# Optimization experiments

Hardware: AMD Instinct MI355X
Metric: run time of the kernel (lower is better)

Reference implementation:

```python
import jax, jax.numpy as jnp
import numpy as np
from jax import lax

EPS_BN = 1e-5
EPS_LN = 1e-5
PATCH = 16

def _gelu(x):
    return jax.nn.gelu(x, approximate=False)

def _patch(x, cw, cb, pw, pb):
    # x: [B, C, H, W]; conv stride=kernel=PATCH -> [B, C, 14, 14]
    y = lax.conv_general_dilated(x, cw, (PATCH, PATCH), 'VALID',
                                 dimension_numbers=('NCHW', 'OIHW', 'NCHW'))
    y = y + cb[None, :, None, None]
    y = y.reshape(y.shape[0], y.shape[1], -1)          # b c (h w) = [B, C, 196]
    return jnp.einsum('bcn,ln->bcl', y, pw) + pb        # Linear(196 -> 256)

def _bn_c(y, g, b, rm, rv):
    # eval-mode BatchNorm over channel axis=1 of [B, C, L]
    inv = g / jnp.sqrt(rv + EPS_BN)
    return y * inv[None, :, None] + (b - rm * inv)[None, :, None]

def _cross(x1, x2, w, b, g, beta, rm, rv):
    c = jnp.concatenate([x1, x2], axis=1)               # [B, 2P, L]
    y = lax.conv_general_dilated(c, w, (1,), ((1, 1),),
                                 dimension_numbers=('NCH', 'OIH', 'NCH'))
    y = y + b[None, :, None]
    return _gelu(_bn_c(y, g, beta, rm, rv))

def _mamba(x, Win, cw, cb, Wx, Wdt, bdt, Alog, Dp, Wout):
    # Standard mamba_ssm Mamba block, eval mode. x: [B, L, D]
    Di = Win.shape[0] // 2
    N = Alog.shape[1]
    R = Wdt.shape[1]
    Bsz, L, _ = x.shape
    xz = jnp.einsum('bld,ed->ble', x, Win)              # in_proj (no bias)
    xc, z = xz[..., :Di], xz[..., Di:]
    K = cw.shape[1]
    xp = jnp.pad(xc, ((0, 0), (K - 1, 0), (0, 0)))      # causal depthwise conv
    xconv = cb + sum(xp[:, k:k + L, :] * cw[:, k] for k in range(K))
    xc = jax.nn.silu(xconv)
    dbc = jnp.einsum('bld,ed->ble', xc, Wx)             # x_proj
    dt = jax.nn.softplus(jnp.einsum('blr,dr->bld', dbc[..., :R], Wdt) + bdt)
    Bm = dbc[..., R:R + N]
    Cm = dbc[..., R + N:]
    A = -jnp.exp(Alog)                                  # [Di, N]
    def step(h, inp):
        dt_t, b_t, c_t, x_t = inp                       # [B,Di],[B,N],[B,N],[B,Di]
        h = jnp.exp(dt_t[:, :, None] * A) * h + dt_t[:, :, None] * b_t[:, None, :] * x_t[:, :, None]
        return h, jnp.einsum('bdn,bn->bd', h, c_t)
    h0 = jnp.zeros((Bsz, Di, N), x.dtype)
    _, ys = lax.scan(step, h0, (dt.swapaxes(0, 1), Bm.swapaxes(0, 1), Cm.swapaxes(0, 1), xc.swapaxes(0, 1)))
    y = ys.swapaxes(0, 1) + Dp * xc
    y = y * jax.nn.silu(z)
    return jnp.einsum('bld,od->blo', y, Wout)           # out_proj (no bias)

def _mamba_stack(x, p):
    # residual stack: x = mamba_i(x) + x
    for i in range(p[0].shape[0]):
        x = _mamba(x, *(q[i] for q in p)) + x
    return x

def _forward(x_cwt, y_cwt, z_cwt,
             x_conv_w, x_conv_b, x_proj_w, x_proj_b,
             y_conv_w, y_conv_b, y_proj_w, y_proj_b,
             z_conv_w, z_conv_b, z_proj_w, z_proj_b,
             cc_w, cc_b, cc_g, cc_beta, cc_rm, cc_rv,
             fu_w, fu_b, fu_g, fu_beta, fu_rm, fu_rv,
             ln_g, ln_b,
             m1_in_w, m1_conv_w, m1_conv_b, m1_x_w, m1_dt_w, m1_dt_b, m1_Alog, m1_D, m1_out_w,
             m2_in_w, m2_conv_w, m2_conv_b, m2_x_w, m2_dt_w, m2_dt_b, m2_Alog, m2_D, m2_out_w,
             cl1_w, cl1_b, cl2_w, cl2_b):
    xr = _gelu(_patch(x_cwt, x_conv_w, x_conv_b, x_proj_w, x_proj_b)).swapaxes(1, 2)  # [B,256,32]
    yr = _gelu(_patch(y_cwt, y_conv_w, y_conv_b, y_proj_w, y_proj_b)).swapaxes(1, 2)
    zr = _gelu(_patch(z_cwt, z_conv_w, z_conv_b, z_proj_w, z_proj_b)).swapaxes(1, 2)
    cxy = _cross(xr, yr, cc_w, cc_b, cc_g, cc_beta, cc_rm, cc_rv)
    cxz = _cross(xr, zr, cc_w, cc_b, cc_g, cc_beta, cc_rm, cc_rv)
    cyz = _cross(yr, zr, cc_w, cc_b, cc_g, cc_beta, cc_rm, cc_rv)
    # max_pooling == 0 -> mean pooling over last dim
    feats = jnp.concatenate([xr.mean(2), yr.mean(2), zr.mean(2),
                             cxy.mean(2), cxz.mean(2), cyz.mean(2)], axis=1)  # [B,1536]
    f = feats @ fu_w.T + fu_b
    inv = fu_g / jnp.sqrt(fu_rv + EPS_BN)
    f = _gelu(f * inv + (fu_beta - fu_rm * inv))        # BN1d eval + GELU (dropout=eval identity)
    xf = f[:, None, :]                                  # [B, 1, 256]
    mu = xf.mean(-1, keepdims=True)
    var = ((xf - mu) ** 2).mean(-1, keepdims=True)
    xf = (xf - mu) / jnp.sqrt(var + EPS_LN) * ln_g + ln_b
    m1 = (m1_in_w, m1_conv_w, m1_conv_b, m1_x_w, m1_dt_w, m1_dt_b, m1_Alog, m1_D, m1_out_w)
    m2 = (m2_in_w, m2_conv_w, m2_conv_b, m2_x_w, m2_dt_w, m2_dt_b, m2_Alog, m2_D, m2_out_w)
    # branch 1: scan over (trivial) time axis, bidirectional, reverse_flip == 1
    x1 = _mamba_stack(xf, m1)
    x1f = _mamba_stack(jnp.flip(xf, axis=1), m1)
    x1 = x1 + jnp.flip(x1f, axis=1)
    # branch 2: scan over feature axis (permuted), bidirectional
    xperm = x1.swapaxes(1, 2)                           # [B, 256, 1]
    x2 = _mamba_stack(xperm, m2)
    x2f = _mamba_stack(jnp.flip(xperm, axis=1), m2)
    x2f = x2f.swapaxes(1, 2)                            # [B, 1, 256]
    x2 = x2.swapaxes(1, 2) + jnp.flip(x2f, axis=1)
    x3 = (x2 + x1)[:, 0, :]                             # squeeze(1)
    h = x3 @ cl1_w.T + cl1_b
    return h @ cl2_w.T + cl2_b

def setup_inputs():
    key = jax.random.key(0)
    ks = iter(jax.random.split(key, 80))
    rn = lambda *s: jax.random.normal(next(ks), s, jnp.float32) * 0.05
    d = {}
    d['x_cwt'] = jax.random.normal(next(ks), (32, 32, 224, 224), jnp.float32)
    d['y_cwt'] = jax.random.normal(next(ks), (32, 32, 224, 224), jnp.float32)
    d['z_cwt'] = jax.random.normal(next(ks), (32, 32, 224, 224), jnp.float32)
    for s in ('x', 'y', 'z'):
        d[s + '_conv_w'] = rn(32, 32, 16, 16)
        d[s + '_conv_b'] = jnp.zeros((32,), jnp.float32)
        d[s + '_proj_w'] = rn(256, 196)
        d[s + '_proj_b'] = jnp.zeros((256,), jnp.float32)
    d['cc_w'] = rn(256, 512, 3); d['cc_b'] = jnp.zeros((256,)); d['cc_g'] = jnp.ones((256,))
    d['cc_beta'] = jnp.zeros((256,)); d['cc_rm'] = jnp.zeros((256,)); d['cc_rv'] = jnp.ones((256,))
    d['fu_w'] = rn(256, 1536); d['fu_b'] = jnp.zeros((256,)); d['fu_g'] = jnp.ones((256,))
    d['fu_beta'] = jnp.zeros((256,)); d['fu_rm'] = jnp.zeros((256,)); d['fu_rv'] = jnp.ones((256,))
    d['ln_g'] = jnp.ones((256,)); d['ln_b'] = jnp.zeros((256,))
    alog = jnp.log(jnp.arange(1, 17, dtype=jnp.float32))
    d['m1_in_w'] = rn(2, 1024, 256); d['m1_conv_w'] = rn(2, 512, 4); d['m1_conv_b'] = jnp.zeros((2, 512))
    d['m1_x_w'] = rn(2, 48, 512); d['m1_dt_w'] = rn(2, 512, 16); d['m1_dt_b'] = jnp.zeros((2, 512))
    d['m1_Alog'] = jnp.broadcast_to(alog, (2, 512, 16)) + 0.0; d['m1_D'] = jnp.ones((2, 512)); d['m1_out_w'] = rn(2, 256, 512)
    d['m2_in_w'] = rn(2, 4, 1); d['m2_conv_w'] = rn(2, 2, 4); d['m2_conv_b'] = jnp.zeros((2, 2))
    d['m2_x_w'] = rn(2, 33, 2); d['m2_dt_w'] = rn(2, 2, 1); d['m2_dt_b'] = jnp.zeros((2, 2))
    d['m2_Alog'] = jnp.broadcast_to(alog, (2, 2, 16)) + 0.0; d['m2_D'] = jnp.ones((2, 2)); d['m2_out_w'] = rn(2, 1, 2)
    d['cl1_w'] = rn(128, 256); d['cl1_b'] = jnp.zeros((128,))
    d['cl2_w'] = rn(18, 128); d['cl2_b'] = jnp.zeros((18,))
    return d

def reference(x_cwt, y_cwt, z_cwt,
              x_conv_w, x_conv_b, x_proj_w, x_proj_b,
              y_conv_w, y_conv_b, y_proj_w, y_proj_b,
              z_conv_w, z_conv_b, z_proj_w, z_proj_b,
              cc_w, cc_b, cc_g, cc_beta, cc_rm, cc_rv,
              fu_w, fu_b, fu_g, fu_beta, fu_rm, fu_rv,
              ln_g, ln_b,
              m1_in_w, m1_conv_w, m1_conv_b, m1_x_w, m1_dt_w, m1_dt_b, m1_Alog, m1_D, m1_out_w,
              m2_in_w, m2_conv_w, m2_conv_b, m2_x_w, m2_dt_w, m2_dt_b, m2_Alog, m2_D, m2_out_w,
              cl1_w, cl1_b, cl2_w, cl2_b):
    return _forward(x_cwt, y_cwt, z_cwt,
                    x_conv_w, x_conv_b, x_proj_w, x_proj_b,
                    y_conv_w, y_conv_b, y_proj_w, y_proj_b,
                    z_conv_w, z_conv_b, z_proj_w, z_proj_b,
                    cc_w, cc_b, cc_g, cc_beta, cc_rm, cc_rv,
                    fu_w, fu_b, fu_g, fu_beta, fu_rm, fu_rv,
                    ln_g, ln_b,
                    m1_in_w, m1_conv_w, m1_conv_b, m1_x_w, m1_dt_w, m1_dt_b, m1_Alog, m1_D, m1_out_w,
                    m2_in_w, m2_conv_w, m2_conv_b, m2_x_w, m2_dt_w, m2_dt_b, m2_Alog, m2_D, m2_out_w,
                    cl1_w, cl1_b, cl2_w, cl2_b)
```

## Files before the change

kernel.cpp:

```cpp
#include <hip/hip_runtime.h>
#include <math.h>


__device__ __forceinline__ float gelu_f(float x) {
    return 0.5f * x * (1.0f + erff(x * 0.70710678118654752f));
}
__device__ __forceinline__ float silu_f(float x) {
    return x / (1.0f + expf(-x));
}
__device__ __forceinline__ float softplus_f(float x) {
    return (x > 20.0f) ? x : log1pf(expf(x));
}

__global__ __launch_bounds__(256, 2)
void k_patch_conv(const float* __restrict__ X0, const float* __restrict__ X1, const float* __restrict__ X2,
                  const float* __restrict__ W0, const float* __restrict__ W1, const float* __restrict__ W2,
                  const float* __restrict__ B0, const float* __restrict__ B1, const float* __restrict__ B2,
                  float* __restrict__ P) {
    int bid = blockIdx.x;
    int s = bid / 448; int rem = bid % 448; int b = rem / 14; int ph = rem % 14;
    const float* X  = (s == 0) ? X0 : ((s == 1) ? X1 : X2);
    const float* W  = (s == 0) ? W0 : ((s == 1) ? W1 : W2);
    const float* Bb = (s == 0) ? B0 : ((s == 1) ? B1 : B2);

    __shared__ float4 xs4[16 * 57];
    __shared__ float4 ws4[32 * 64];
    __shared__ float  red[16 * 112];

    int tid = threadIdx.x;
    int ij = tid & 3;
    int i  = ij & 1;
    int j  = ij >> 1;
    int k  = tid >> 2;
    int kh = k >> 2;
    int kwq = k & 3;

    float acc[7][16];
#pragma unroll
    for (int p = 0; p < 7; ++p) {
#pragma unroll
        for (int c = 0; c < 16; ++c) acc[p][c] = 0.f;
    }

    for (int ci = 0; ci < 32; ++ci) {
        __syncthreads();
        const float4* xg = (const float4*)(X + ((size_t)(b * 32 + ci)) * 50176 + (size_t)ph * 3584);
        for (int t = tid; t < 896; t += 256) {
            int r = t / 56, c4 = t % 56;
            xs4[r * 57 + c4] = xg[t];
        }
        const float4* wg = (const float4*)W;
        for (int t = tid; t < 2048; t += 256) {
            int co = t >> 6, q = t & 63;
            ws4[t] = wg[(size_t)(co * 32 + ci) * 64 + q];
        }
        __syncthreads();

        float4 xv[7];
        const float4* xr_ = &xs4[kh * 57 + i * 28 + kwq];
#pragma unroll
        for (int p = 0; p < 7; ++p) xv[p] = xr_[p * 4];
#pragma unroll
        for (int c = 0; c < 16; ++c) {
            float4 wv = ws4[(j * 16 + c) * 64 + k];
#pragma unroll
            for (int p = 0; p < 7; ++p) {
                acc[p][c] += xv[p].x * wv.x + xv[p].y * wv.y + xv[p].z * wv.z + xv[p].w * wv.w;
            }
        }
    }

#pragma unroll
    for (int p = 0; p < 7; ++p) {
#pragma unroll
        for (int c = 0; c < 16; ++c) {
            float v = acc[p][c];
            v += __shfl_xor(v, 4);
            v += __shfl_xor(v, 8);
            v += __shfl_xor(v, 16);
            v += __shfl_xor(v, 32);
            acc[p][c] = v;
        }
    }
    int wave = tid >> 6, lane = tid & 63;
    if (lane < 4) {
#pragma unroll
        for (int p = 0; p < 7; ++p) {
#pragma unroll
            for (int c = 0; c < 16; ++c) {
                red[(wave * 4 + lane) * 112 + p * 16 + c] = acc[p][c];
            }
        }
    }
    __syncthreads();
    for (int t = tid; t < 448; t += 256) {
        int ij2 = t / 112, v = t % 112;
        int p = v / 16, c = v % 16;
        float sum = red[(0 * 4 + ij2) * 112 + v] + red[(1 * 4 + ij2) * 112 + v] +
                    red[(2 * 4 + ij2) * 112 + v] + red[(3 * 4 + ij2) * 112 + v];
        int pw = (ij2 & 1) * 7 + p;
        int co = (ij2 >> 1) * 16 + c;
        P[(((size_t)s * 32 + b) * 32 + co) * 196 + ph * 14 + pw] = sum + Bb[co];
    }
}

__global__ __launch_bounds__(128)
void k_proj(const float* __restrict__ P,
            const float* __restrict__ PW0, const float* __restrict__ PW1, const float* __restrict__ PW2,
            const float* __restrict__ PB0, const float* __restrict__ PB1, const float* __restrict__ PB2,
            float* __restrict__ R, float* __restrict__ feats) {
    int bid = blockIdx.x;
    int s = bid / 64; int r2 = bid % 64; int b = r2 >> 1; int half = r2 & 1;
    const float* PW = (s == 0) ? PW0 : ((s == 1) ? PW1 : PW2);
    const float* PB = (s == 0) ? PB0 : ((s == 1) ? PB1 : PB2);

    __shared__ float4 ps4[32 * 49];
    const float4* src = (const float4*)(P + ((size_t)s * 32 + b) * 6272);
    for (int t = threadIdx.x; t < 1568; t += 128) ps4[t] = src[t];
    __syncthreads();

    int l = half * 128 + threadIdx.x;
    float acc[32];
#pragma unroll
    for (int c = 0; c < 32; ++c) acc[c] = 0.f;

    const float4* pwl = (const float4*)(PW + (size_t)l * 196);
    for (int n4 = 0; n4 < 49; ++n4) {
        float4 pv = pwl[n4];
#pragma unroll
        for (int c = 0; c < 32; ++c) {
            float4 xv = ps4[c * 49 + n4];
            acc[c] += pv.x * xv.x + pv.y * xv.y + pv.z * xv.z + pv.w * xv.w;
        }
    }
    float pbl = PB[l];
    float m = 0.f;
    float* Rrow = R + (((size_t)s * 32 + b) * 256 + l) * 32;
#pragma unroll
    for (int c = 0; c < 32; ++c) {
        float v = gelu_f(acc[c] + pbl);
        Rrow[c] = v;
        m += v;
    }
    feats[b * 1536 + s * 256 + l] = m * 0.03125f;
}

__global__ __launch_bounds__(256)
void k_cross(const float* __restrict__ R, const float* __restrict__ CCW,
             const float* __restrict__ CCB, const float* __restrict__ CCG,
             const float* __restrict__ CCBETA, const float* __restrict__ CCRM,
             const float* __restrict__ CCRV, float* __restrict__ feats) {
    int b = blockIdx.x >> 3, cs = blockIdx.x & 7;
    int c0 = cs * 4;
    __shared__ float ls[3 * 256 * 8];
    for (int t = threadIdx.x; t < 4608; t += 256) {
        int ten = t / 1536; int r2 = t % 1536; int r = r2 / 6; int cc = r2 % 6;
        int cg = c0 - 1 + cc;
        float v = 0.f;
        if (cg >= 0 && cg < 32) v = R[(((size_t)ten * 32 + b) * 256 + r) * 32 + cg];
        ls[(ten * 256 + r) * 8 + cc] = v;
    }
    __syncthreads();

    int o = threadIdx.x;
    float a1[4] = {0, 0, 0, 0}, a2[4] = {0, 0, 0, 0}, a3[4] = {0, 0, 0, 0};
    const float* wrow = CCW + (size_t)o * 1536;

    for (int ii = 0; ii < 256; ++ii) {
        float w0 = wrow[ii * 3], w1 = wrow[ii * 3 + 1], w2 = wrow[ii * 3 + 2];
        const float* U = &ls[(0 * 256 + ii) * 8];
        const float* V = &ls[(1 * 256 + ii) * 8];
#pragma unroll
        for (int c = 0; c < 4; ++c) {
            float su_ = w0 * U[c] + w1 * U[c + 1] + w2 * U[c + 2];
            float sv_ = w0 * V[c] + w1 * V[c + 1] + w2 * V[c + 2];
            a1[c] += su_; a2[c] += su_; a3[c] += sv_;
        }
    }
    for (int ii = 0; ii < 256; ++ii) {
        float w0 = wrow[768 + ii * 3], w1 = wrow[768 + ii * 3 + 1], w2 = wrow[768 + ii * 3 + 2];
        const float* U = &ls[(1 * 256 + ii) * 8];
        const float* V = &ls[(2 * 256 + ii) * 8];
#pragma unroll
        for (int c = 0; c < 4; ++c) {
            float su_ = w0 * U[c] + w1 * U[c + 1] + w2 * U[c + 2];
            float sv_ = w0 * V[c] + w1 * V[c + 1] + w2 * V[c + 2];
            a1[c] += su_; a2[c] += sv_; a3[c] += sv_;
        }
    }

    float inv = CCG[o] / sqrtf(CCRV[o] + 1e-5f);
    float sh = CCBETA[o] - CCRM[o] * inv;
    float bias = CCB[o];
    float s1 = 0.f, s2 = 0.f, s3 = 0.f;
#pragma unroll
    for (int c = 0; c < 4; ++c) {
        s1 += gelu_f((a1[c] + bias) * inv + sh);
        s2 += gelu_f((a2[c] + bias) * inv + sh);
        s3 += gelu_f((a3[c] + bias) * inv + sh);
    }
    float* fb = feats + b * 1536 + 768;
    atomicAdd(&fb[o],       s1 * 0.03125f);
    atomicAdd(&fb[256 + o], s2 * 0.03125f);
    atomicAdd(&fb[512 + o], s3 * 0.03125f);
}

__global__ __launch_bounds__(256)
void k_fuse(const float* __restrict__ feats, const float* __restrict__ FUW, const float* __restrict__ FUB,
            const float* __restrict__ FUG, const float* __restrict__ FUBETA, const float* __restrict__ FURM,
            const float* __restrict__ FURV, const float* __restrict__ LNG, const float* __restrict__ LNB,
            float* __restrict__ xf) {
    int b = blockIdx.x;
    __shared__ float4 sf4[384];
    const float4* src = (const float4*)(feats + (size_t)b * 1536);
    for (int t = threadIdx.x; t < 384; t += 256) sf4[t] = src[t];
    __syncthreads();

    int o = threadIdx.x;
    const float4* wr = (const float4*)(FUW + (size_t)o * 1536);
    float acc = 0.f;
    for (int q = 0; q < 384; ++q) {
        float4 wv = wr[q], xv = sf4[q];
        acc += wv.x * xv.x + wv.y * xv.y + wv.z * xv.z + wv.w * xv.w;
    }
    float inv = FUG[o] / sqrtf(FURV[o] + 1e-5f);
    float f = (acc + FUB[o]) * inv + (FUBETA[o] - FURM[o] * inv);
    f = gelu_f(f);

    float s1 = f, s2 = f * f;
#pragma unroll
    for (int off = 32; off >= 1; off >>= 1) {
        s1 += __shfl_xor(s1, off);
        s2 += __shfl_xor(s2, off);
    }
    __shared__ float wred[8];
    int wave = threadIdx.x >> 6, lane = threadIdx.x & 63;
    if (lane == 0) { wred[wave * 2] = s1; wred[wave * 2 + 1] = s2; }
    __syncthreads();
    float mu  = (wred[0] + wred[2] + wred[4] + wred[6]) * (1.f / 256.f);
    float ex2 = (wred[1] + wred[3] + wred[5] + wred[7]) * (1.f / 256.f);
    float var = ex2 - mu * mu;
    xf[b * 256 + o] = (f - mu) / sqrtf(var + 1e-5f) * LNG[o] + LNB[o];
}

__global__ __launch_bounds__(256)
void k_m1(const float* __restrict__ Uin, float* __restrict__ Uout,
          const float* __restrict__ WIN, const float* __restrict__ CW, const float* __restrict__ CB,
          const float* __restrict__ WX, const float* __restrict__ WDT, const float* __restrict__ BDT,
          const float* __restrict__ DP, const float* __restrict__ WOUT, int layer) {
    const float* Win  = WIN  + (size_t)layer * 1024 * 256;
    const float* cw   = CW   + layer * 2048;
    const float* cb   = CB   + layer * 512;
    const float* Wx   = WX   + layer * 48 * 512;
    const float* Wdt  = WDT  + layer * 512 * 16;
    const float* bdt  = BDT  + layer * 512;
    const float* Dp   = DP   + layer * 512;
    const float* Wout = WOUT + layer * 256 * 512;

    int b = blockIdx.x, tid = threadIdx.x;
    __shared__ float su[256];
    __shared__ float sz[1024];
    __shared__ float sx[512];
    __shared__ float sdbc[48];
    __shared__ float sy[512];

    su[tid] = Uin[b * 256 + tid];
    __syncthreads();

    const float4* su4 = (const float4*)su;
#pragma unroll
    for (int q = 0; q < 4; ++q) {
        int e = tid + q * 256;
        const float4* wr = (const float4*)(Win + (size_t)e * 256);
        float acc = 0.f;
        for (int t = 0; t < 64; ++t) {
            float4 wv = wr[t], xv = su4[t];
            acc += wv.x * xv.x + wv.y * xv.y + wv.z * xv.z + wv.w * xv.w;
        }
        sz[e] = acc;
    }
    __syncthreads();
#pragma unroll
    for (int q = 0; q < 2; ++q) {
        int d = tid + q * 256;
        sx[d] = silu_f(cb[d] + sz[d] * cw[d * 4 + 3]);
    }
    __syncthreads();
    if (tid < 48) {
        const float4* wr = (const float4*)(Wx + (size_t)tid * 512);
        const float4* sx4 = (const float4*)sx;
        float acc = 0.f;
        for (int t = 0; t < 128; ++t) {
            float4 wv = wr[t], xv = sx4[t];
            acc += wv.x * xv.x + wv.y * xv.y + wv.z * xv.z + wv.w * xv.w;
        }
        sdbc[tid] = acc;
    }
    __syncthreads();
    float bc = 0.f;
#pragma unroll
    for (int n = 0; n < 16; ++n) bc += sdbc[16 + n] * sdbc[32 + n];
#pragma unroll
    for (int q = 0; q < 2; ++q) {
        int d = tid + q * 256;
        float dtin = 0.f;
#pragma unroll
        for (int r = 0; r < 16; ++r) dtin += sdbc[r] * Wdt[d * 16 + r];
        float dtv = softplus_f(dtin + bdt[d]);
        float xcv = sx[d];
        float y = dtv * xcv * bc + Dp[d] * xcv;
        y *= silu_f(sz[512 + d]);
        sy[d] = y;
    }
    __syncthreads();
    {
        const float4* wr = (const float4*)(Wout + (size_t)tid * 512);
        const float4* sy4 = (const float4*)sy;
        float acc = 0.f;
        for (int t = 0; t < 128; ++t) {
            float4 wv = wr[t], xv = sy4[t];
            acc += wv.x * xv.x + wv.y * xv.y + wv.z * xv.z + wv.w * xv.w;
        }
        Uout[b * 256 + tid] = acc + su[tid];
    }
}

__global__ __launch_bounds__(256)
void k_m2(const float* __restrict__ SRC, float* __restrict__ DST, int first,
          const float* __restrict__ WIN, const float* __restrict__ CW, const float* __restrict__ CB,
          const float* __restrict__ WX, const float* __restrict__ WDT, const float* __restrict__ BDT,
          const float* __restrict__ ALOG, const float* __restrict__ DP, const float* __restrict__ WOUT,
          int layer) {
    const float* Win  = WIN  + layer * 4;
    const float* cw   = CW   + layer * 8;
    const float* cb   = CB   + layer * 2;
    const float* Wx   = WX   + layer * 66;
    const float* Wdt  = WDT  + layer * 2;
    const float* bdt  = BDT  + layer * 2;
    const float* Alog = ALOG + layer * 32;
    const float* Dp   = DP   + layer * 2;
    const float* Wout = WOUT + layer * 2;

    int v = blockIdx.x, b = v >> 1, dir = v & 1, l = threadIdx.x;
    __shared__ float sxc[256 * 2];
    __shared__ float sC[256 * 16];
    __shared__ float suu[256 * 32];
    __shared__ float sdt[256 * 2];
    __shared__ float sy[256 * 2];

    float u;
    if (first) u = 2.f * SRC[b * 256 + (dir ? (255 - l) : l)];
    else       u = SRC[v * 256 + l];

    float xc0 = u * Win[0], xc1 = u * Win[1];
    float z0  = u * Win[2], z1  = u * Win[3];
    sxc[l * 2 + 0] = xc0; sxc[l * 2 + 1] = xc1;
    __syncthreads();

    float xs0, xs1;
    {
        float a0 = cb[0], a1 = cb[1];
#pragma unroll
        for (int kk = 0; kk < 4; ++kk) {
            int lk = l - 3 + kk;
            if (lk >= 0) {
                a0 += sxc[lk * 2 + 0] * cw[kk];
                a1 += sxc[lk * 2 + 1] * cw[4 + kk];
            }
        }
        xs0 = silu_f(a0); xs1 = silu_f(a1);
    }
    float dbc0 = xs0 * Wx[0] + xs1 * Wx[1];
    float dt0 = softplus_f(dbc0 * Wdt[0] + bdt[0]);
    float dt1 = softplus_f(dbc0 * Wdt[1] + bdt[1]);
    sdt[l * 2 + 0] = dt0; sdt[l * 2 + 1] = dt1;
#pragma unroll
    for (int n = 0; n < 16; ++n) {
        float Bn = xs0 * Wx[(1 + n) * 2] + xs1 * Wx[(1 + n) * 2 + 1];
        float Cn = xs0 * Wx[(17 + n) * 2] + xs1 * Wx[(17 + n) * 2 + 1];
        sC[l * 16 + n] = Cn;
        suu[l * 32 + n]      = dt0 * Bn * xs0;
        suu[l * 32 + 16 + n] = dt1 * Bn * xs1;
    }
    __syncthreads();

    if (l < 32) {
        int d = l >> 4, n = l & 15;
        float A = -expf(Alog[d * 16 + n]);
        float h = 0.f;
#pragma unroll 4
        for (int t = 0; t < 256; ++t) {
            float a = expf(sdt[t * 2 + d] * A);
            h = a * h + suu[t * 32 + l];
            float part = h * sC[t * 16 + n];
            part += __shfl_xor(part, 1);
            part += __shfl_xor(part, 2);
            part += __shfl_xor(part, 4);
            part += __shfl_xor(part, 8);
            if (n == 0) sy[t * 2 + d] = part;
        }
    }
    __syncthreads();
    {
        float y0 = sy[l * 2 + 0] + Dp[0] * xs0;
        float y1 = sy[l * 2 + 1] + Dp[1] * xs1;
        y0 *= silu_f(z0); y1 *= silu_f(z1);
        DST[v * 256 + l] = y0 * Wout[0] + y1 * Wout[1] + u;
    }
}

__global__ __launch_bounds__(256)
void k_final(const float* __restrict__ M2b, const float* __restrict__ XF1,
             const float* __restrict__ CL1W, const float* __restrict__ CL1B,
             const float* __restrict__ CL2W, const float* __restrict__ CL2B,
             float* __restrict__ out) {
    int b = blockIdx.x, tid = threadIdx.x;
    __shared__ float sx3[256];
    __shared__ float shh[128];
    sx3[tid] = M2b[(2 * b) * 256 + tid] + M2b[(2 * b + 1) * 256 + tid] + 2.f * XF1[b * 256 + tid];
    __syncthreads();
    if (tid < 128) {
        const float4* wr = (const float4*)(CL1W + (size_t)tid * 256);
        const float4* x4 = (const float4*)sx3;
        float acc = 0.f;
        for (int t = 0; t < 64; ++t) {
            float4 wv = wr[t], xv = x4[t];
            acc += wv.x * xv.x + wv.y * xv.y + wv.z * xv.z + wv.w * xv.w;
        }
        shh[tid] = acc + CL1B[tid];
    }
    __syncthreads();
    if (tid < 18) {
        const float4* wr = (const float4*)(CL2W + (size_t)tid * 128);
        const float4* h4 = (const float4*)shh;
        float acc = 0.f;
        for (int t = 0; t < 32; ++t) {
            float4 wv = wr[t], xv = h4[t];
            acc += wv.x * xv.x + wv.y * xv.y + wv.z * xv.z + wv.w * xv.w;
        }
        out[b * 18 + tid] = acc + CL2B[tid];
    }
}


#define DI(i) ((const float*)d_in[i])

extern "C" void kernel_launch(void* const* d_in, const int* in_sizes, int n_in,
                              void* d_out, int out_size, void* d_ws, size_t ws_size,
                              hipStream_t stream) {
    float* ws    = (float*)d_ws;
    float* P     = ws;
    float* R     = P + 602112;
    float* feats = R + 786432;
    float* xf    = feats + 49152;
    float* U1    = xf + 8192;
    float* XF1   = U1 + 8192;
    float* M2a   = XF1 + 8192;
    float* M2b   = M2a + 16384;

    hipMemsetAsync(feats, 0, 49152 * sizeof(float), stream);

    k_patch_conv<<<1344, 256, 0, stream>>>(DI(0), DI(1), DI(2),
                                           DI(3), DI(7), DI(11),
                                           DI(4), DI(8), DI(12), P);
    k_proj<<<192, 128, 0, stream>>>(P, DI(5), DI(9), DI(13), DI(6), DI(10), DI(14), R, feats);
    k_cross<<<256, 256, 0, stream>>>(R, DI(15), DI(16), DI(17), DI(18), DI(19), DI(20), feats);
    k_fuse<<<32, 256, 0, stream>>>(feats, DI(21), DI(22), DI(23), DI(24), DI(25), DI(26),
                                   DI(27), DI(28), xf);
    k_m1<<<32, 256, 0, stream>>>(xf, U1, DI(29), DI(30), DI(31), DI(32), DI(33), DI(34),
                                 DI(36), DI(37), 0);
    k_m1<<<32, 256, 0, stream>>>(U1, XF1, DI(29), DI(30), DI(31), DI(32), DI(33), DI(34),
                                 DI(36), DI(37), 1);
    k_m2<<<64, 256, 0, stream>>>(XF1, M2a, 1, DI(38), DI(39), DI(40), DI(41), DI(42), DI(43),
                                 DI(44), DI(45), DI(46), 0);
    k_m2<<<64, 256, 0, stream>>>(M2a, M2b, 0, DI(38), DI(39), DI(40), DI(41), DI(42), DI(43),
                                 DI(44), DI(45), DI(46), 1);
    k_final<<<32, 256, 0, stream>>>(M2b, XF1, DI(47), DI(48), DI(49), DI(50), (float*)d_out);
}
```

Before: 1.439 ms.

## Double-buffer patch conv via direct global-to-LDS loads and pretranspose weights for coalescing

```diff
diff --git a/kernel.cpp b/kernel.cpp
--- a/kernel.cpp
+++ b/kernel.cpp
@@ -10,6 +10,40 @@
 }
 __device__ __forceinline__ float softplus_f(float x) {
     return (x > 20.0f) ? x : log1pf(expf(x));
+}
+
+__device__ __forceinline__ void gl2lds(const float4* g, float4* l) {
+    __builtin_amdgcn_global_load_lds((const __attribute__((address_space(1))) void*)g,
+                                     (__attribute__((address_space(3))) void*)l,
+                                     16, 0, 0);
+}
+
+__global__ __launch_bounds__(256)
+void k_tr(const float* __restrict__ src, float* __restrict__ dst, int R, int C) {
+    __shared__ float t[32][33];
+    int ctiles = C >> 5;
+    int bx = blockIdx.x % ctiles, by = blockIdx.x / ctiles;
+    int c0 = bx * 32, r0 = by * 32;
+    int tx = threadIdx.x & 31, ty = threadIdx.x >> 5;
+#pragma unroll
+    for (int k = 0; k < 4; ++k) {
+        int r = ty + k * 8;
+        t[r][tx] = src[(size_t)(r0 + r) * C + c0 + tx];
+    }
+    __syncthreads();
+#pragma unroll
+    for (int k = 0; k < 4; ++k) {
+        int r = ty + k * 8;
+        dst[(size_t)(c0 + r) * R + r0 + tx] = t[tx][r];
+    }
+}
+
+__global__ __launch_bounds__(256)
+void k_p4(const float* __restrict__ src, float4* __restrict__ dst, int E, int Dq) {
+    int idx = blockIdx.x * 256 + threadIdx.x;
+    if (idx >= E * Dq) return;
+    int e = idx / Dq, dq = idx % Dq;
+    dst[(size_t)dq * E + e] = *(const float4*)(src + (size_t)e * 4 * Dq + 4 * dq);
 }
 
 __global__ __launch_bounds__(256, 2)
@@ -23,11 +57,12 @@
     const float* W  = (s == 0) ? W0 : ((s == 1) ? W1 : W2);
     const float* Bb = (s == 0) ? B0 : ((s == 1) ? B1 : B2);
 
-    __shared__ float4 xs4[16 * 57];
-    __shared__ float4 ws4[32 * 64];
+    __shared__ float4 xs4[2][1024];
+    __shared__ float4 ws4[2048];
     __shared__ float  red[16 * 112];
 
     int tid = threadIdx.x;
+    int wave = tid >> 6, lane = tid & 63;
     int ij = tid & 3;
     int i  = ij & 1;
     int j  = ij >> 1;
@@ -35,29 +70,45 @@
     int kh = k >> 2;
     int kwq = k & 3;
 
+    const float4* xg = (const float4*)X + (size_t)(b * 32) * 12544 + ph * 896;
+    const float4* wg = (const float4*)W;
+
+#pragma unroll
+    for (int q = 0; q < 4; ++q) {
+        int chunk = wave * 4 + q;
+        int idx = chunk * 64 + lane; if (idx > 895) idx = 895;
+        gl2lds(xg + idx, &xs4[0][chunk * 64]);
+    }
+
     float acc[7][16];
 #pragma unroll
-    for (int p = 0; p < 7; ++p) {
+    for (int p = 0; p < 7; ++p)
 #pragma unroll
         for (int c = 0; c < 16; ++c) acc[p][c] = 0.f;
-    }
 
     for (int ci = 0; ci < 32; ++ci) {
-        __syncthreads();
-        const float4* xg = (const float4*)(X + ((size_t)(b * 32 + ci)) * 50176 + (size_t)ph * 3584);
-        for (int t = tid; t < 896; t += 256) {
-            int r = t / 56, c4 = t % 56;
-            xs4[r * 57 + c4] = xg[t];
-        }
-        const float4* wg = (const float4*)W;
-        for (int t = tid; t < 2048; t += 256) {
-            int co = t >> 6, q = t & 63;
-            ws4[t] = wg[(size_t)(co * 32 + ci) * 64 + q];
-        }
-        __syncthreads();
-
+        asm volatile("s_barrier" ::: "memory");
+#pragma unroll
+        for (int q = 0; q < 8; ++q) {
+            int c = wave * 8 + q;
+            gl2lds(wg + (size_t)c * 2048 + ci * 64 + lane, &ws4[c * 64]);
+        }
+        if (ci < 31) {
+            const float4* xgn = xg + (size_t)(ci + 1) * 12544;
+#pragma unroll
+            for (int q = 0; q < 4; ++q) {
+                int chunk = wave * 4 + q;
+                int idx = chunk * 64 + lane; if (idx > 895) idx = 895;
+                gl2lds(xgn + idx, &xs4[(ci + 1) & 1][chunk * 64]);
+            }
+            asm volatile("s_waitcnt vmcnt(4)" ::: "memory");
+        } else {
+            asm volatile("s_waitcnt vmcnt(0)" ::: "memory");
+        }
+        asm volatile("s_barrier" ::: "memory");
+
+        const float4* xr_ = &xs4[ci & 1][kh * 56 + i * 28 + kwq];
         float4 xv[7];
-        const float4* xr_ = &xs4[kh * 57 + i * 28 + kwq];
 #pragma unroll
         for (int p = 0; p < 7; ++p) xv[p] = xr_[p * 4];
 #pragma unroll
@@ -82,15 +133,12 @@
             acc[p][c] = v;
         }
     }
-    int wave = tid >> 6, lane = tid & 63;
     if (lane < 4) {
 #pragma unroll
-        for (int p = 0; p < 7; ++p) {
-#pragma unroll
-            for (int c = 0; c < 16; ++c) {
+        for (int p = 0; p < 7; ++p)
+#pragma unroll
+            for (int c = 0; c < 16; ++c)
                 red[(wave * 4 + lane) * 112 + p * 16 + c] = acc[p][c];
-            }
-        }
     }
     __syncthreads();
     for (int t = tid; t < 448; t += 256) {
@@ -105,16 +153,15 @@
 }
 
 __global__ __launch_bounds__(128)
-void k_proj(const float* __restrict__ P,
-            const float* __restrict__ PW0, const float* __restrict__ PW1, const float* __restrict__ PW2,
+void k_proj(const float* __restrict__ P, const float4* __restrict__ PWP,
             const float* __restrict__ PB0, const float* __restrict__ PB1, const float* __restrict__ PB2,
             float* __restrict__ R, float* __restrict__ feats) {
     int bid = blockIdx.x;
     int s = bid / 64; int r2 = bid % 64; int b = r2 >> 1; int half = r2 & 1;
-    const float* PW = (s == 0) ? PW0 : ((s == 1) ? PW1 : PW2);
     const float* PB = (s == 0) ? PB0 : ((s == 1) ? PB1 : PB2);
-
-    __shared__ float4 ps4[32 * 49];
+    const float4* pwp = PWP + (size_t)s * 12544;
+
+    __shared__ __align__(16) float4 ps4[32 * 49];
     const float4* src = (const float4*)(P + ((size_t)s * 32 + b) * 6272);
     for (int t = threadIdx.x; t < 1568; t += 128) ps4[t] = src[t];
     __syncthreads();
@@ -124,9 +171,8 @@
 #pragma unroll
     for (int c = 0; c < 32; ++c) acc[c] = 0.f;
 
-    const float4* pwl = (const float4*)(PW + (size_t)l * 196);
     for (int n4 = 0; n4 < 49; ++n4) {
-        float4 pv = pwl[n4];
+        float4 pv = pwp[n4 * 256 + l];
 #pragma unroll
         for (int c = 0; c < 32; ++c) {
             float4 xv = ps4[c * 49 + n4];
@@ -146,13 +192,13 @@
 }
 
 __global__ __launch_bounds__(256)
-void k_cross(const float* __restrict__ R, const float* __restrict__ CCW,
+void k_cross(const float* __restrict__ R, const float* __restrict__ CCWT,
              const float* __restrict__ CCB, const float* __restrict__ CCG,
              const float* __restrict__ CCBETA, const float* __restrict__ CCRM,
              const float* __restrict__ CCRV, float* __restrict__ feats) {
     int b = blockIdx.x >> 3, cs = blockIdx.x & 7;
     int c0 = cs * 4;
-    __shared__ float ls[3 * 256 * 8];
+    __shared__ __align__(16) float ls[3 * 256 * 8];
     for (int t = threadIdx.x; t < 4608; t += 256) {
         int ten = t / 1536; int r2 = t % 1536; int r = r2 / 6; int cc = r2 % 6;
         int cg = c0 - 1 + cc;
@@ -164,29 +210,46 @@
 
     int o = threadIdx.x;
     float a1[4] = {0, 0, 0, 0}, a2[4] = {0, 0, 0, 0}, a3[4] = {0, 0, 0, 0};
-    const float* wrow = CCW + (size_t)o * 1536;
 
     for (int ii = 0; ii < 256; ++ii) {
-        float w0 = wrow[ii * 3], w1 = wrow[ii * 3 + 1], w2 = wrow[ii * 3 + 2];
+        float w0 = CCWT[(ii * 3 + 0) * 256 + o];
+        float w1 = CCWT[(ii * 3 + 1) * 256 + o];
+        float w2 = CCWT[(ii * 3 + 2) * 256 + o];
         const float* U = &ls[(0 * 256 + ii) * 8];
         const float* V = &ls[(1 * 256 + ii) * 8];
-#pragma unroll
-        for (int c = 0; c < 4; ++c) {
-            float su_ = w0 * U[c] + w1 * U[c + 1] + w2 * U[c + 2];
-            float sv_ = w0 * V[c] + w1 * V[c + 1] + w2 * V[c + 2];
-            a1[c] += su_; a2[c] += su_; a3[c] += sv_;
-        }
+        float4 ua = *(const float4*)U; float2 ub = *(const float2*)(U + 4);
+        float4 va = *(const float4*)V; float2 vb = *(const float2*)(V + 4);
+        float s0 = w0 * ua.x + w1 * ua.y + w2 * ua.z;
+        float s1 = w0 * ua.y + w1 * ua.z + w2 * ua.w;
+        float s2 = w0 * ua.z + w1 * ua.w + w2 * ub.x;
+        float s3 = w0 * ua.w + w1 * ub.x + w2 * ub.y;
+        float t0 = w0 * va.x + w1 * va.y + w2 * va.z;
+        float t1 = w0 * va.y + w1 * va.z + w2 * va.w;
+        float t2 = w0 * va.z + w1 * va.w + w2 * vb.x;
+        float t3 = w0 * va.w + w1 * vb.x + w2 * vb.y;
+        a1[0] += s0; a1[1] += s1; a1[2] += s2; a1[3] += s3;
+        a2[0] += s0; a2[1] += s1; a2[2] += s2; a2[3] += s3;
+        a3[0] += t0; a3[1] += t1; a3[2] += t2; a3[3] += t3;
     }
     for (int ii = 0; ii < 256; ++ii) {
-        float w0 = wrow[768 + ii * 3], w1 = wrow[768 + ii * 3 + 1], w2 = wrow[768 + ii * 3 + 2];
+        float w0 = CCWT[(768 + ii * 3 + 0) * 256 + o];
+        float w1 = CCWT[(768 + ii * 3 + 1) * 256 + o];
+        float w2 = CCWT[(768 + ii * 3 + 2) * 256 + o];
         const float* U = &ls[(1 * 256 + ii) * 8];
         const float* V = &ls[(2 * 256 + ii) * 8];
-#pragma unroll
-        for (int c = 0; c < 4; ++c) {
-            float su_ = w0 * U[c] + w1 * U[c + 1] + w2 * U[c + 2];
-            float sv_ = w0 * V[c] + w1 * V[c + 1] + w2 * V[c + 2];
-            a1[c] += su_; a2[c] += sv_; a3[c] += sv_;
-        }
+        float4 ua = *(const float4*)U; float2 ub = *(const float2*)(U + 4);
+        float4 va = *(const float4*)V; float2 vb = *(const float2*)(V + 4);
+        float s0 = w0 * ua.x + w1 * ua.y + w2 * ua.z;
+        float s1 = w0 * ua.y + w1 * ua.z + w2 * ua.w;
+        float s2 = w0 * ua.z + w1 * ua.w + w2 * ub.x;
+        float s3 = w0 * ua.w + w1 * ub.x + w2 * ub.y;
+        float t0 = w0 * va.x + w1 * va.y + w2 * va.z;
+        float t1 = w0 * va.y + w1 * va.z + w2 * va.w;
+        float t2 = w0 * va.z + w1 * va.w + w2 * vb.x;
+        float t3 = w0 * va.w + w1 * vb.x + w2 * vb.y;
+        a1[0] += s0; a1[1] += s1; a1[2] += s2; a1[3] += s3;
+        a2[0] += t0; a2[1] += t1; a2[2] += t2; a2[3] += t3;
+        a3[0] += t0; a3[1] += t1; a3[2] += t2; a3[3] += t3;
     }
 
     float inv = CCG[o] / sqrtf(CCRV[o] + 1e-5f);
@@ -206,21 +269,21 @@
 }
 
 __global__ __launch_bounds__(256)
-void k_fuse(const float* __restrict__ feats, const float* __restrict__ FUW, const float* __restrict__ FUB,
+void k_fuse(const float* __restrict__ feats, const float4* __restrict__ FUWP, const float* __restrict__ FUB,
             const float* __restrict__ FUG, const float* __restrict__ FUBETA, const float* __restrict__ FURM,
             const float* __restrict__ FURV, const float* __restrict__ LNG, const float* __restrict__ LNB,
             float* __restrict__ xf) {
     int b = blockIdx.x;
-    __shared__ float4 sf4[384];
+    __shared__ __align__(16) float4 sf4[384];
     const float4* src = (const float4*)(feats + (size_t)b * 1536);
     for (int t = threadIdx.x; t < 384; t += 256) sf4[t] = src[t];
     __syncthreads();
 
     int o = threadIdx.x;
-    const float4* wr = (const float4*)(FUW + (size_t)o * 1536);
     float acc = 0.f;
-    for (int q = 0; q < 384; ++q) {
-        float4 wv = wr[q], xv = sf4[q];
+    for (int kq = 0; kq < 384; ++kq) {
+        float4 wv = FUWP[kq * 256 + o];
+        float4 xv = sf4[kq];
         acc += wv.x * xv.x + wv.y * xv.y + wv.z * xv.z + wv.w * xv.w;
     }
     float inv = FUG[o] / sqrtf(FURV[o] + 1e-5f);
@@ -245,39 +308,38 @@
 
 __global__ __launch_bounds__(256)
 void k_m1(const float* __restrict__ Uin, float* __restrict__ Uout,
-          const float* __restrict__ WIN, const float* __restrict__ CW, const float* __restrict__ CB,
-          const float* __restrict__ WX, const float* __restrict__ WDT, const float* __restrict__ BDT,
-          const float* __restrict__ DP, const float* __restrict__ WOUT, int layer) {
-    const float* Win  = WIN  + (size_t)layer * 1024 * 256;
+          const float4* __restrict__ WinP, const float* __restrict__ CW, const float* __restrict__ CB,
+          const float* __restrict__ WX, const float4* __restrict__ WdtP, const float* __restrict__ BDT,
+          const float* __restrict__ DP, const float4* __restrict__ WoutP, int layer) {
     const float* cw   = CW   + layer * 2048;
     const float* cb   = CB   + layer * 512;
     const float* Wx   = WX   + layer * 48 * 512;
-    const float* Wdt  = WDT  + layer * 512 * 16;
     const float* bdt  = BDT  + layer * 512;
     const float* Dp   = DP   + layer * 512;
-    const float* Wout = WOUT + layer * 256 * 512;
 
     int b = blockIdx.x, tid = threadIdx.x;
-    __shared__ float su[256];
-    __shared__ float sz[1024];
-    __shared__ float sx[512];
-    __shared__ float sdbc[48];
-    __shared__ float sy[512];
+    __shared__ __align__(16) float su[256];
+    __shared__ __align__(16) float sz[1024];
+    __shared__ __align__(16) float sx[512];
+    __shared__ __align__(16) float sdbc[48];
+    __shared__ __align__(16) float sy[512];
 
     su[tid] = Uin[b * 256 + tid];
     __syncthreads();
 
     const float4* su4 = (const float4*)su;
-#pragma unroll
-    for (int q = 0; q < 4; ++q) {
-        int e = tid + q * 256;
-        const float4* wr = (const float4*)(Win + (size_t)e * 256);
-        float acc = 0.f;
-        for (int t = 0; t < 64; ++t) {
-            float4 wv = wr[t], xv = su4[t];
-            acc += wv.x * xv.x + wv.y * xv.y + wv.z * xv.z + wv.w * xv.w;
-        }
-        sz[e] = acc;
+    {
+        float accq[4] = {0.f, 0.f, 0.f, 0.f};
+        for (int dq = 0; dq < 64; ++dq) {
+            float4 s4 = su4[dq];
+#pragma unroll
+            for (int q = 0; q < 4; ++q) {
+                float4 w4 = WinP[dq * 2048 + layer * 1024 + q * 256 + tid];
+                accq[q] += w4.x * s4.x + w4.y * s4.y + w4.z * s4.z + w4.w * s4.w;
+            }
+        }
+#pragma unroll
+        for (int q = 0; q < 4; ++q) sz[tid + q * 256] = accq[q];
     }
     __syncthreads();
 #pragma unroll
@@ -300,12 +362,17 @@
     float bc = 0.f;
 #pragma unroll
     for (int n = 0; n < 16; ++n) bc += sdbc[16 + n] * sdbc[32 + n];
+    const float4* sdbc4 = (const float4*)sdbc;
 #pragma unroll
     for (int q = 0; q < 2; ++q) {
         int d = tid + q * 256;
         float dtin = 0.f;
 #pragma unroll
-        for (int r = 0; r < 16; ++r) dtin += sdbc[r] * Wdt[d * 16 + r];
+        for (int rq = 0; rq < 4; ++rq) {
+            float4 w4 = WdtP[rq * 1024 + layer * 512 + d];
+            float4 s4 = sdbc4[rq];
+            dtin += w4.x * s4.x + w4.y * s4.y + w4.z * s4.z + w4.w * s4.w;
+        }
         float dtv = softplus_f(dtin + bdt[d]);
         float xcv = sx[d];
         float y = dtv * xcv * bc + Dp[d] * xcv;
@@ -314,12 +381,12 @@
     }
     __syncthreads();
     {
-        const float4* wr = (const float4*)(Wout + (size_t)tid * 512);
         const float4* sy4 = (const float4*)sy;
         float acc = 0.f;
-        for (int t = 0; t < 128; ++t) {
-            float4 wv = wr[t], xv = sy4[t];
-            acc += wv.x * xv.x + wv.y * xv.y + wv.z * xv.z + wv.w * xv.w;
+        for (int dq = 0; dq < 128; ++dq) {
+            float4 w4 = WoutP[dq * 512 + layer * 256 + tid];
+            float4 s4 = sy4[dq];
+            acc += w4.x * s4.x + w4.y * s4.y + w4.z * s4.z + w4.w * s4.w;
         }
         Uout[b * 256 + tid] = acc + su[tid];
     }
@@ -415,8 +482,8 @@
              const float* __restrict__ CL2W, const float* __restrict__ CL2B,
              float* __restrict__ out) {
     int b = blockIdx.x, tid = threadIdx.x;
-    __shared__ float sx3[256];
-    __shared__ float shh[128];
+    __shared__ __align__(16) float sx3[256];
+    __shared__ __align__(16) float shh[128];
     sx3[tid] = M2b[(2 * b) * 256 + tid] + M2b[(2 * b + 1) * 256 + tid] + 2.f * XF1[b * 256 + tid];
     __syncthreads();
     if (tid < 128) {
@@ -457,20 +524,35 @@
     float* XF1   = U1 + 8192;
     float* M2a   = XF1 + 8192;
     float* M2b   = M2a + 16384;
+    float* CCWT  = M2b + 16384;
+    float* FUWP  = CCWT + 393216;
+    float* WinP  = FUWP + 393216;
+    float* WdtP  = WinP + 524288;
+    float* WoutP = WdtP + 16384;
+    float* PWP   = WoutP + 262144;
 
     hipMemsetAsync(feats, 0, 49152 * sizeof(float), stream);
+
+    k_tr<<<384, 256, 0, stream>>>(DI(15), CCWT, 256, 1536);
+    k_p4<<<49,  256, 0, stream>>>(DI(5),  (float4*)(PWP),          256, 49);
+    k_p4<<<49,  256, 0, stream>>>(DI(9),  (float4*)(PWP + 50176),  256, 49);
+    k_p4<<<49,  256, 0, stream>>>(DI(13), (float4*)(PWP + 100352), 256, 49);
+    k_p4<<<384, 256, 0, stream>>>(DI(21), (float4*)FUWP,  256,  384);
+    k_p4<<<512, 256, 0, stream>>>(DI(29), (float4*)WinP,  2048, 64);
+    k_p4<<<16,  256, 0, stream>>>(DI(33), (float4*)WdtP,  1024, 4);
+    k_p4<<<256, 256, 0, stream>>>(DI(37), (float4*)WoutP, 512,  128);
 
     k_patch_conv<<<1344, 256, 0, stream>>>(DI(0), DI(1), DI(2),
                                            DI(3), DI(7), DI(11),
                                            DI(4), DI(8), DI(12), P);
-    k_proj<<<192, 128, 0, stream>>>(P, DI(5), DI(9), DI(13), DI(6), DI(10), DI(14), R, feats);
-    k_cross<<<256, 256, 0, stream>>>(R, DI(15), DI(16), DI(17), DI(18), DI(19), DI(20), feats);
-    k_fuse<<<32, 256, 0, stream>>>(feats, DI(21), DI(22), DI(23), DI(24), DI(25), DI(26),
-                                   DI(27), DI(28), xf);
-    k_m1<<<32, 256, 0, stream>>>(xf, U1, DI(29), DI(30), DI(31), DI(32), DI(33), DI(34),
-                                 DI(36), DI(37), 0);
-    k_m1<<<32, 256, 0, stream>>>(U1, XF1, DI(29), DI(30), DI(31), DI(32), DI(33), DI(34),
-                                 DI(36), DI(37), 1);
+    k_proj<<<192, 128, 0, stream>>>(P, (const float4*)PWP, DI(6), DI(10), DI(14), R, feats);
+    k_cross<<<256, 256, 0, stream>>>(R, CCWT, DI(16), DI(17), DI(18), DI(19), DI(20), feats);
+    k_fuse<<<32, 256, 0, stream>>>(feats, (const float4*)FUWP, DI(22), DI(23), DI(24), DI(25),
+                                   DI(26), DI(27), DI(28), xf);
+    k_m1<<<32, 256, 0, stream>>>(xf, U1, (const float4*)WinP, DI(30), DI(31), DI(32),
+                                 (const float4*)WdtP, DI(34), DI(36), (const float4*)WoutP, 0);
+    k_m1<<<32, 256, 0, stream>>>(U1, XF1, (const float4*)WinP, DI(30), DI(31), DI(32),
+                                 (const float4*)WdtP, DI(34), DI(36), (const float4*)WoutP, 1);
     k_m2<<<64, 256, 0, stream>>>(XF1, M2a, 1, DI(38), DI(39), DI(40), DI(41), DI(42), DI(43),
                                  DI(44), DI(45), DI(46), 0);
     k_m2<<<64, 256, 0, stream>>>(M2a, M2b, 0, DI(38), DI(39), DI(40), DI(41), DI(42), DI(43),
```

New measurement: 1.215 ms. -15.6%, faster.
